# Performance work log

Hardware: AMD Instinct MI355X
Metric: run time of the kernel (lower is better)

The kernel has to match this reference:

```python
import jax, jax.numpy as jnp
import numpy as np


def setup_inputs() -> dict:
    key = jax.random.key(0)
    kq, kk, kv = jax.random.split(key, 3)
    B, H, T, D = 2, 8, 8192, 64
    return {
        "Q": jax.random.normal(kq, (B, H, T, D), dtype=jnp.float32),
        "K": jax.random.normal(kk, (B, H, T, D), dtype=jnp.float32),
        "V": jax.random.normal(kv, (B, H, T, D), dtype=jnp.float32),
        "window_size": 512,
    }


def _gather_bands(x, nb, Wn):
    # x: [B,H,T,D] -> [B,H,nb,3*Wn,D], key blocks (i-1, i, i+1) per query block i
    B, H, T, D = x.shape
    xb = x.reshape(B, H, nb, Wn, D)
    xp = jnp.pad(xb, ((0, 0), (0, 0), (1, 1), (0, 0), (0, 0)))
    return jnp.concatenate([xp[:, :, i:i + nb] for i in range(3)], axis=3)


def reference(Q, K, V, window_size):
    # Sliding-window attention: softmax over keys with |q_idx - kv_idx| <= window_size,
    # computed block-sparsely (only the 3 neighboring key blocks per query block).
    B, H, T, D = Q.shape
    Wn = int(window_size)
    assert T % Wn == 0
    nb = T // Wn
    scale = 1.0 / (D ** 0.5)

    Qb = Q.reshape(B, H, nb, Wn, D)
    Kw = _gather_bands(K, nb, Wn)  # [B,H,nb,3W,D]
    Vw = _gather_bands(V, nb, Wn)

    # scores within the band: [B,H,nb,W,3W]
    s = jnp.einsum('bhnqd,bhnkd->bhnqk', Qb, Kw) * scale

    # exact band mask: global q = n*W + q_loc, global kv = (n-1)*W + k_loc
    q_loc = jnp.arange(Wn)[:, None]
    k_loc = jnp.arange(3 * Wn)[None, :]
    band = jnp.abs(q_loc + Wn - k_loc) <= Wn          # [W, 3W]
    kv_g = (jnp.arange(nb)[:, None] - 1) * Wn + jnp.arange(3 * Wn)[None, :]  # [nb, 3W]
    valid = (kv_g >= 0) & (kv_g < T)
    mask = band[None, :, :] & valid[:, None, :]        # [nb, W, 3W]

    s = jnp.where(mask[None, None], s, -jnp.inf)
    p = jax.nn.softmax(s, axis=-1)
    o = jnp.einsum('bhnqk,bhnkd->bhnqd', p, Vw)
    return o.reshape(B, H, T, D)
```

## Files before the change

kernel.cpp:

```cpp
#include <hip/hip_runtime.h>
#include <hip/hip_bf16.h>
#include <stdint.h>

typedef __attribute__((ext_vector_type(8))) short bf16x8;
typedef __attribute__((ext_vector_type(4))) short bf16x4;
typedef __attribute__((ext_vector_type(4))) float f32x4;

#define T_SEQ   8192
#define D_HEAD  64
#define NHEADS  16
#define WIN     512
#define BQ      128
#define BK      64
#define NTILES  (T_SEQ / BK)
#define LDSR    72
#define MASKVAL (-1.0e6f)

#define WS_NEEDED ((size_t)2 * NHEADS * T_SEQ * D_HEAD * 2)

#define MFMA16(a,b,c) __builtin_amdgcn_mfma_f32_16x16x16bf16_1k(a,b,c,0,0,0)

extern "C" __device__ __attribute__((const)) float __ocml_native_exp2_f32(float);
__device__ __forceinline__ float fexp2(float x) { return __ocml_native_exp2_f32(x); }

__device__ __forceinline__ short f2bf(float f) {
    union { float f; uint32_t u; } v; v.f = f;
    return (short)((v.u + 0x7FFFu + ((v.u >> 16) & 1u)) >> 16);
}

__device__ __forceinline__ uint32_t pkbf2(float lo, float hi) {
    union { __hip_bfloat162 h; uint32_t u; } c;
    c.h = __float22bfloat162_rn(make_float2(lo, hi));
    return c.u;
}

__global__ __launch_bounds__(256, 2)
void prep_kv(const float* __restrict__ Kg, const float* __restrict__ Vg,
             short* __restrict__ Kb, short* __restrict__ Vt)
{
    __shared__ float vt[64 * 65];
    const int tid  = threadIdx.x;
    const int tile = blockIdx.x & (NTILES - 1);
    const int head = blockIdx.x >> 7;
    const size_t off = ((size_t)head * T_SEQ + (size_t)tile * BK) * D_HEAD;

    const float* ks = Kg + off;
    short* kd = Kb + off;
    #pragma unroll
    for (int i = 0; i < 4; ++i) {
        int idx = tid + 256 * i;
        float4 v = *(const float4*)(ks + idx * 4);
        short4 h = { f2bf(v.x), f2bf(v.y), f2bf(v.z), f2bf(v.w) };
        *(short4*)(kd + idx * 4) = h;
    }

    const float* vs = Vg + off;
    #pragma unroll
    for (int i = 0; i < 4; ++i) {
        int idx = tid + 256 * i;
        int row = idx >> 4, c4 = (idx & 15) << 2;
        float4 v = *(const float4*)(vs + row * D_HEAD + c4);
        *(float4*)&vt[row * 65 + c4] = v;
    }
    __syncthreads();
    short* vd = Vt + ((size_t)head * NTILES + tile) * (BK * D_HEAD);
    {
        int d = tid >> 2, kq = (tid & 3) << 4;
        short out[16];
        #pragma unroll
        for (int j = 0; j < 16; ++j) out[j] = f2bf(vt[(kq + j) * 65 + d]);
        *(bf16x8*)(vd + d * BK + kq)     = *(bf16x8*)&out[0];
        *(bf16x8*)(vd + d * BK + kq + 8) = *(bf16x8*)&out[8];
    }
}

__global__ __launch_bounds__(256, 4)
void swa_fwd(const float* __restrict__ Qg, const short* __restrict__ Kb,
             const short* __restrict__ Vt, float* __restrict__ Og)
{
    __shared__ short Ks[2][BK * LDSR];
    __shared__ short Vs[2][BK * LDSR];

    const int tid  = threadIdx.x;
    const int wave = tid >> 6;
    const int lane = tid & 63;
    const int lcol = lane & 15;
    const int quad = lane >> 4;

    const int g    = blockIdx.x;
    const int head = g >> 6;
    const int qt   = ((g & 7) << 3) | ((g >> 3) & 7);
    const int q0   = qt * BQ;
    const int tq   = q0 >> 6;

    const float* Qp = Qg + (size_t)head * T_SEQ * D_HEAD;
    const short* Kp = Kb + (size_t)head * T_SEQ * D_HEAD;
    float*       Op = Og + (size_t)head * T_SEQ * D_HEAD;

    const float qscale = 0.125f * 1.44269504088896340736f;
    const int qrow_w = q0 + wave * 32;

    bf16x8 qf[2][2];
    #pragma unroll
    for (int mt = 0; mt < 2; ++mt) {
        const float* qptr = Qp + (size_t)(qrow_w + mt*16 + lcol) * D_HEAD + quad * 8;
        #pragma unroll
        for (int ks = 0; ks < 2; ++ks) {
            float4 a = *(const float4*)(qptr + ks*32);
            float4 b = *(const float4*)(qptr + ks*32 + 4);
            bf16x8 f;
            f[0]=f2bf(a.x*qscale); f[1]=f2bf(a.y*qscale); f[2]=f2bf(a.z*qscale); f[3]=f2bf(a.w*qscale);
            f[4]=f2bf(b.x*qscale); f[5]=f2bf(b.y*qscale); f[6]=f2bf(b.z*qscale); f[7]=f2bf(b.w*qscale);
            qf[mt][ks] = f;
        }
    }

    f32x4 oacc[2][4];
    float l_run[2];
    const f32x4 zero4 = {0.f, 0.f, 0.f, 0.f};
    #pragma unroll
    for (int mt = 0; mt < 2; ++mt) {
        l_run[mt] = 0.f;
        #pragma unroll
        for (int nt = 0; nt < 4; ++nt) oacc[mt][nt] = zero4;
    }

    int t0 = (q0 - WIN) >> 6;            if (t0 < 0) t0 = 0;
    int t1 = (q0 + BQ - 1 + WIN) >> 6;   if (t1 > NTILES - 1) t1 = NTILES - 1;

    const int srow0 = tid >> 3, sc0 = (tid & 7) << 3;
    const int srow1 = srow0 + 32;
    const int sOff0 = srow0 * LDSR + sc0;
    const int sOff1 = srow1 * LDSR + sc0;

    {
        const short* ksrc = Kp + (size_t)t0 * BK * D_HEAD;
        const short* vsrc = Vt + ((size_t)head * NTILES + t0) * (BK * D_HEAD);
        *(bf16x8*)&Ks[0][sOff0] = *(const bf16x8*)(ksrc + tid * 8);
        *(bf16x8*)&Ks[0][sOff1] = *(const bf16x8*)(ksrc + (tid + 256) * 8);
        *(bf16x8*)&Vs[0][sOff0] = *(const bf16x8*)(vsrc + tid * 8);
        *(bf16x8*)&Vs[0][sOff1] = *(const bf16x8*)(vsrc + (tid + 256) * 8);
    }
    bf16x8 k0, k1, v0, v1;
    {
        const int tn = (t0 + 1 <= t1) ? t0 + 1 : t1;
        const short* ksrc = Kp + (size_t)tn * BK * D_HEAD;
        const short* vsrc = Vt + ((size_t)head * NTILES + tn) * (BK * D_HEAD);
        k0 = *(const bf16x8*)(ksrc + tid * 8);
        k1 = *(const bf16x8*)(ksrc + (tid + 256) * 8);
        v0 = *(const bf16x8*)(vsrc + tid * 8);
        v1 = *(const bf16x8*)(vsrc + (tid + 256) * 8);
    }
    __syncthreads();

    int p = 0;
    for (int t = t0; t <= t1; ++t) {
        *(bf16x8*)&Ks[p^1][sOff0] = k0;
        *(bf16x8*)&Ks[p^1][sOff1] = k1;
        *(bf16x8*)&Vs[p^1][sOff0] = v0;
        *(bf16x8*)&Vs[p^1][sOff1] = v1;

        {
            const int tn = (t + 2 <= t1) ? t + 2 : t1;
            const short* ksrc = Kp + (size_t)tn * BK * D_HEAD;
            const short* vsrc = Vt + ((size_t)head * NTILES + tn) * (BK * D_HEAD);
            k0 = *(const bf16x8*)(ksrc + tid * 8);
            k1 = *(const bf16x8*)(ksrc + (tid + 256) * 8);
            v0 = *(const bf16x8*)(vsrc + tid * 8);
            v1 = *(const bf16x8*)(vsrc + (tid + 256) * 8);
        }

        const short* Kcur = Ks[p];
        const short* Vcur = Vs[p];
        const bool edge = (t < tq - 6) || (t > tq + 7);

        #pragma unroll
        for (int h = 0; h < 2; ++h) {
            f32x4 sc[2][2];
            #pragma unroll
            for (int j = 0; j < 2; ++j) { sc[j][0] = zero4; sc[j][1] = zero4; }
            #pragma unroll
            for (int ks = 0; ks < 2; ++ks) {
                #pragma unroll
                for (int j = 0; j < 2; ++j) {
                    bf16x8 kf = *(const bf16x8*)&Kcur[((2*h+j)*16 + lcol)*LDSR + ks*32 + quad*8];
                    sc[j][0] = __builtin_amdgcn_mfma_f32_16x16x32_bf16(kf, qf[0][ks], sc[j][0], 0,0,0);
                    sc[j][1] = __builtin_amdgcn_mfma_f32_16x16x32_bf16(kf, qf[1][ks], sc[j][1], 0,0,0);
                }
            }

            if (edge) {
                #pragma unroll
                for (int j = 0; j < 2; ++j) {
                    const int kg0 = t*BK + (2*h+j)*16 + quad*4;
                    #pragma unroll
                    for (int mt = 0; mt < 2; ++mt) {
                        const int qg = qrow_w + mt*16 + lcol;
                        #pragma unroll
                        for (int r = 0; r < 4; ++r) {
                            int dq = qg - (kg0 + r);
                            if (dq > WIN || dq < -WIN) sc[j][mt][r] = MASKVAL;
                        }
                    }
                }
            }

            #pragma unroll
            for (int j = 0; j < 2; ++j) {
                const int kt = 2*h + j;
                bf16x4 vf[4];
                #pragma unroll
                for (int nt = 0; nt < 4; ++nt)
                    vf[nt] = *(const bf16x4*)&Vcur[(nt*16 + lcol)*LDSR + kt*16 + quad*4];
                #pragma unroll
                for (int mt = 0; mt < 2; ++mt) {
                    float p0 = fexp2(sc[j][mt][0]);
                    float p1 = fexp2(sc[j][mt][1]);
                    float p2 = fexp2(sc[j][mt][2]);
                    float p3 = fexp2(sc[j][mt][3]);
                    l_run[mt] += (p0 + p1) + (p2 + p3);
                    union { int2 i; bf16x4 v; } pf;
                    pf.i = make_int2((int)pkbf2(p0, p1), (int)pkbf2(p2, p3));
                    #pragma unroll
                    for (int nt = 0; nt < 4; ++nt)
                        oacc[mt][nt] = MFMA16(vf[nt], pf.v, oacc[mt][nt]);
                }
            }
        }

        __syncthreads();
        p ^= 1;
    }

    #pragma unroll
    for (int mt = 0; mt < 2; ++mt) {
        float l = l_run[mt];
        l += __shfl_xor(l, 16, 64);
        l += __shfl_xor(l, 32, 64);
        float inv = 1.0f / l;
        const int qg = qrow_w + mt*16 + lcol;
        float* op = Op + (size_t)qg * D_HEAD + quad*4;
        #pragma unroll
        for (int nt = 0; nt < 4; ++nt) {
            float4 o = { oacc[mt][nt][0]*inv, oacc[mt][nt][1]*inv,
                         oacc[mt][nt][2]*inv, oacc[mt][nt][3]*inv };
            *(float4*)(op + nt*16) = o;
        }
    }
}

#define BQF     128
__global__ __launch_bounds__(256, 4)
void swa_fused_fb(const float* __restrict__ Qg, const float* __restrict__ Kg,
                  const float* __restrict__ Vg, float* __restrict__ Og)
{
    __shared__ short Ksf[BK * LDSR];
    __shared__ short Vsf[D_HEAD * LDSR];
    __shared__ float Vtmp[BK * 65];

    const int tid  = threadIdx.x;
    const int wave = tid >> 6;
    const int lane = tid & 63;
    const int lcol = lane & 15;
    const int quad = lane >> 4;

    const int g    = blockIdx.x;
    const int head = g >> 6;
    const int qt   = ((g & 7) << 3) | ((g >> 3) & 7);
    const int q0   = qt * BQF;
    const int tq   = q0 >> 6;

    const size_t hoff = (size_t)head * T_SEQ * D_HEAD;
    const float* Qp = Qg + hoff;
    const float* Kp = Kg + hoff;
    const float* Vp = Vg + hoff;
    float*       Op = Og + hoff;

    const float qscale = 0.125f * 1.44269504088896340736f;
    const int qrow_w = q0 + wave * 32;

    bf16x8 qf[2][2];
    #pragma unroll
    for (int mt = 0; mt < 2; ++mt) {
        const float* qptr = Qp + (size_t)(qrow_w + mt*16 + lcol) * D_HEAD + quad * 8;
        #pragma unroll
        for (int ks = 0; ks < 2; ++ks) {
            float4 a = *(const float4*)(qptr + ks*32);
            float4 b = *(const float4*)(qptr + ks*32 + 4);
            bf16x8 f;
            f[0]=f2bf(a.x*qscale); f[1]=f2bf(a.y*qscale); f[2]=f2bf(a.z*qscale); f[3]=f2bf(a.w*qscale);
            f[4]=f2bf(b.x*qscale); f[5]=f2bf(b.y*qscale); f[6]=f2bf(b.z*qscale); f[7]=f2bf(b.w*qscale);
            qf[mt][ks] = f;
        }
    }

    f32x4 oacc[2][4];
    float l_run[2];
    const f32x4 zero4 = {0.f, 0.f, 0.f, 0.f};
    #pragma unroll
    for (int mt = 0; mt < 2; ++mt) {
        l_run[mt] = 0.f;
        #pragma unroll
        for (int nt = 0; nt < 4; ++nt) oacc[mt][nt] = zero4;
    }

    int t0 = (q0 - WIN) >> 6;            if (t0 < 0) t0 = 0;
    int t1 = (q0 + BQF - 1 + WIN) >> 6;  if (t1 > NTILES - 1) t1 = NTILES - 1;

    const int krow0 = tid >> 3, kc = (tid & 7) << 3;
    const int krow1 = krow0 + 32;
    const int vrow  = tid >> 4, vc = (tid & 15) << 2;
    const int td    = tid >> 2, tkq = (tid & 3) << 4;

    for (int t = t0; t <= t1; ++t) {
        const float* ksrc = Kp + (size_t)t * BK * D_HEAD;
        const float* vsrc = Vp + (size_t)t * BK * D_HEAD;
        float4 k00 = *(const float4*)(ksrc + krow0*D_HEAD + kc);
        float4 k01 = *(const float4*)(ksrc + krow0*D_HEAD + kc + 4);
        float4 k10 = *(const float4*)(ksrc + krow1*D_HEAD + kc);
        float4 k11 = *(const float4*)(ksrc + krow1*D_HEAD + kc + 4);
        float4 v0  = *(const float4*)(vsrc + (vrow     )*D_HEAD + vc);
        float4 v1  = *(const float4*)(vsrc + (vrow + 16)*D_HEAD + vc);
        float4 v2  = *(const float4*)(vsrc + (vrow + 32)*D_HEAD + vc);
        float4 v3  = *(const float4*)(vsrc + (vrow + 48)*D_HEAD + vc);

        __syncthreads();

        *(float4*)&Vtmp[(vrow     )*65 + vc] = v0;
        *(float4*)&Vtmp[(vrow + 16)*65 + vc] = v1;
        *(float4*)&Vtmp[(vrow + 32)*65 + vc] = v2;
        *(float4*)&Vtmp[(vrow + 48)*65 + vc] = v3;
        *(int4*)&Ksf[krow0*LDSR + kc] = make_int4((int)pkbf2(k00.x,k00.y), (int)pkbf2(k00.z,k00.w),
                                                  (int)pkbf2(k01.x,k01.y), (int)pkbf2(k01.z,k01.w));
        *(int4*)&Ksf[krow1*LDSR + kc] = make_int4((int)pkbf2(k10.x,k10.y), (int)pkbf2(k10.z,k10.w),
                                                  (int)pkbf2(k11.x,k11.y), (int)pkbf2(k11.z,k11.w));

        __syncthreads();

        {
            uint32_t w0 = pkbf2(Vtmp[(tkq+ 0)*65 + td], Vtmp[(tkq+ 1)*65 + td]);
            uint32_t w1 = pkbf2(Vtmp[(tkq+ 2)*65 + td], Vtmp[(tkq+ 3)*65 + td]);
            uint32_t w2 = pkbf2(Vtmp[(tkq+ 4)*65 + td], Vtmp[(tkq+ 5)*65 + td]);
            uint32_t w3 = pkbf2(Vtmp[(tkq+ 6)*65 + td], Vtmp[(tkq+ 7)*65 + td]);
            uint32_t w4 = pkbf2(Vtmp[(tkq+ 8)*65 + td], Vtmp[(tkq+ 9)*65 + td]);
            uint32_t w5 = pkbf2(Vtmp[(tkq+10)*65 + td], Vtmp[(tkq+11)*65 + td]);
            uint32_t w6 = pkbf2(Vtmp[(tkq+12)*65 + td], Vtmp[(tkq+13)*65 + td]);
            uint32_t w7 = pkbf2(Vtmp[(tkq+14)*65 + td], Vtmp[(tkq+15)*65 + td]);
            *(int4*)&Vsf[td*LDSR + tkq]     = make_int4((int)w0,(int)w1,(int)w2,(int)w3);
            *(int4*)&Vsf[td*LDSR + tkq + 8] = make_int4((int)w4,(int)w5,(int)w6,(int)w7);
        }

        __syncthreads();

        const bool edge = (t < tq - 6) || (t > tq + 7);

        #pragma unroll
        for (int h = 0; h < 2; ++h) {
            f32x4 sc[2][2];
            #pragma unroll
            for (int j = 0; j < 2; ++j) { sc[j][0] = zero4; sc[j][1] = zero4; }
            #pragma unroll
            for (int ks = 0; ks < 2; ++ks) {
                #pragma unroll
                for (int j = 0; j < 2; ++j) {
                    bf16x8 kf = *(const bf16x8*)&Ksf[((2*h+j)*16 + lcol)*LDSR + ks*32 + quad*8];
                    sc[j][0] = __builtin_amdgcn_mfma_f32_16x16x32_bf16(kf, qf[0][ks], sc[j][0], 0,0,0);
                    sc[j][1] = __builtin_amdgcn_mfma_f32_16x16x32_bf16(kf, qf[1][ks], sc[j][1], 0,0,0);
                }
            }

            if (edge) {
                #pragma unroll
                for (int j = 0; j < 2; ++j) {
                    const int kg0 = t*BK + (2*h+j)*16 + quad*4;
                    #pragma unroll
                    for (int mt = 0; mt < 2; ++mt) {
                        const int qg = qrow_w + mt*16 + lcol;
                        #pragma unroll
                        for (int r = 0; r < 4; ++r) {
                            int dq = qg - (kg0 + r);
                            if (dq > WIN || dq < -WIN) sc[j][mt][r] = MASKVAL;
                        }
                    }
                }
            }

            #pragma unroll
            for (int j = 0; j < 2; ++j) {
                const int kt = 2*h + j;
                bf16x4 vf[4];
                #pragma unroll
                for (int nt = 0; nt < 4; ++nt)
                    vf[nt] = *(const bf16x4*)&Vsf[(nt*16 + lcol)*LDSR + kt*16 + quad*4];
                #pragma unroll
                for (int mt = 0; mt < 2; ++mt) {
                    float p0 = fexp2(sc[j][mt][0]);
                    float p1 = fexp2(sc[j][mt][1]);
                    float p2 = fexp2(sc[j][mt][2]);
                    float p3 = fexp2(sc[j][mt][3]);
                    l_run[mt] += (p0 + p1) + (p2 + p3);
                    union { int2 i; bf16x4 v; } pf;
                    pf.i = make_int2((int)pkbf2(p0, p1), (int)pkbf2(p2, p3));
                    #pragma unroll
                    for (int nt = 0; nt < 4; ++nt)
                        oacc[mt][nt] = MFMA16(vf[nt], pf.v, oacc[mt][nt]);
                }
            }
        }
    }

    #pragma unroll
    for (int mt = 0; mt < 2; ++mt) {
        float l = l_run[mt];
        l += __shfl_xor(l, 16, 64);
        l += __shfl_xor(l, 32, 64);
        float inv = 1.0f / l;
        const int qg = qrow_w + mt*16 + lcol;
        float* op = Op + (size_t)qg * D_HEAD + quad*4;
        #pragma unroll
        for (int nt = 0; nt < 4; ++nt) {
            float4 o = { oacc[mt][nt][0]*inv, oacc[mt][nt][1]*inv,
                         oacc[mt][nt][2]*inv, oacc[mt][nt][3]*inv };
            *(float4*)(op + nt*16) = o;
        }
    }
}

extern "C" void kernel_launch(void* const* d_in, const int* in_sizes, int n_in,
                              void* d_out, int out_size, void* d_ws, size_t ws_size,
                              hipStream_t stream)
{
    const float* Q = (const float*)d_in[0];
    const float* K = (const float*)d_in[1];
    const float* V = (const float*)d_in[2];
    float* O = (float*)d_out;

    if (ws_size >= WS_NEEDED) {
        short* Kb = (short*)d_ws;
        short* Vt = Kb + (size_t)NHEADS * T_SEQ * D_HEAD;
        prep_kv<<<dim3(NHEADS * NTILES), dim3(256), 0, stream>>>(K, V, Kb, Vt);
        swa_fwd<<<dim3(NHEADS * (T_SEQ / BQ)), dim3(256), 0, stream>>>(Q, Kb, Vt, O);
    } else {
        swa_fused_fb<<<dim3(NHEADS * (T_SEQ / BQF)), dim3(256), 0, stream>>>(Q, K, V, O);
    }
}
```

Before: 204.5 us.

## Load K/V tiles directly into LDS with XOR-swizzled layout

Replaces the register-staged global→LDS copy of the K and V tiles with direct global_load_lds transfers, using a one-tile-ahead double-buffer pipeline. The prep kernel now writes K and V^T with an XOR swizzle on 16-byte chunks, and the LDS reads undo it. This removes the padded LDS rows while avoiding bank conflicts. The goal is to cut VGPR pressure and LDS store instructions. The risk is shallower prefetch, since distance drops from two tiles to one, plus a full vmcnt(0) wait before every barrier.

```diff
diff --git a/kernel.cpp b/kernel.cpp
--- a/kernel.cpp
+++ b/kernel.cpp
@@ -23,6 +23,10 @@
 extern "C" __device__ __attribute__((const)) float __ocml_native_exp2_f32(float);
 __device__ __forceinline__ float fexp2(float x) { return __ocml_native_exp2_f32(x); }
 
+#define GLDS16(g, l) __builtin_amdgcn_global_load_lds( \
+    (const __attribute__((address_space(1))) void*)(g), \
+    (__attribute__((address_space(3))) void*)(l), 16, 0, 0)
+
 __device__ __forceinline__ short f2bf(float f) {
     union { float f; uint32_t u; } v; v.f = f;
     return (short)((v.u + 0x7FFFu + ((v.u >> 16) & 1u)) >> 16);
@@ -47,11 +51,15 @@
     const float* ks = Kg + off;
     short* kd = Kb + off;
     #pragma unroll
-    for (int i = 0; i < 4; ++i) {
-        int idx = tid + 256 * i;
-        float4 v = *(const float4*)(ks + idx * 4);
-        short4 h = { f2bf(v.x), f2bf(v.y), f2bf(v.z), f2bf(v.w) };
-        *(short4*)(kd + idx * 4) = h;
+    for (int i = 0; i < 2; ++i) {
+        int L = tid + 256 * i;
+        int row = L >> 3, c = L & 7;
+        const float* s = ks + row * 64 + c * 8;
+        float4 a = *(const float4*)s;
+        float4 b = *(const float4*)(s + 4);
+        short out[8] = { f2bf(a.x), f2bf(a.y), f2bf(a.z), f2bf(a.w),
+                         f2bf(b.x), f2bf(b.y), f2bf(b.z), f2bf(b.w) };
+        *(bf16x8*)(kd + (row * 8 + (c ^ (row & 7))) * 8) = *(bf16x8*)out;
     }
 
     const float* vs = Vg + off;
@@ -66,11 +74,12 @@
     short* vd = Vt + ((size_t)head * NTILES + tile) * (BK * D_HEAD);
     {
         int d = tid >> 2, kq = (tid & 3) << 4;
+        int c = kq >> 3;
         short out[16];
         #pragma unroll
         for (int j = 0; j < 16; ++j) out[j] = f2bf(vt[(kq + j) * 65 + d]);
-        *(bf16x8*)(vd + d * BK + kq)     = *(bf16x8*)&out[0];
-        *(bf16x8*)(vd + d * BK + kq + 8) = *(bf16x8*)&out[8];
+        *(bf16x8*)(vd + (d * 8 + ( c      ^ (d & 7))) * 8) = *(bf16x8*)&out[0];
+        *(bf16x8*)(vd + (d * 8 + ((c + 1) ^ (d & 7))) * 8) = *(bf16x8*)&out[8];
     }
 }
 
@@ -78,14 +87,15 @@
 void swa_fwd(const float* __restrict__ Qg, const short* __restrict__ Kb,
              const short* __restrict__ Vt, float* __restrict__ Og)
 {
-    __shared__ short Ks[2][BK * LDSR];
-    __shared__ short Vs[2][BK * LDSR];
+    __shared__ short Ks[2][BK * D_HEAD];
+    __shared__ short Vs[2][BK * D_HEAD];
 
     const int tid  = threadIdx.x;
     const int wave = tid >> 6;
     const int lane = tid & 63;
     const int lcol = lane & 15;
     const int quad = lane >> 4;
+    const int rx   = lcol & 7;
 
     const int g    = blockIdx.x;
     const int head = g >> 6;
@@ -128,50 +138,35 @@
     int t0 = (q0 - WIN) >> 6;            if (t0 < 0) t0 = 0;
     int t1 = (q0 + BQ - 1 + WIN) >> 6;   if (t1 > NTILES - 1) t1 = NTILES - 1;
 
-    const int srow0 = tid >> 3, sc0 = (tid & 7) << 3;
-    const int srow1 = srow0 + 32;
-    const int sOff0 = srow0 * LDSR + sc0;
-    const int sOff1 = srow1 * LDSR + sc0;
+    const int ch0 = wave * 2, ch1 = wave * 2 + 1;
 
     {
-        const short* ksrc = Kp + (size_t)t0 * BK * D_HEAD;
+        const short* ksrc = Kp + (size_t)t0 * (BK * D_HEAD);
         const short* vsrc = Vt + ((size_t)head * NTILES + t0) * (BK * D_HEAD);
-        *(bf16x8*)&Ks[0][sOff0] = *(const bf16x8*)(ksrc + tid * 8);
-        *(bf16x8*)&Ks[0][sOff1] = *(const bf16x8*)(ksrc + (tid + 256) * 8);
-        *(bf16x8*)&Vs[0][sOff0] = *(const bf16x8*)(vsrc + tid * 8);
-        *(bf16x8*)&Vs[0][sOff1] = *(const bf16x8*)(vsrc + (tid + 256) * 8);
-    }
-    bf16x8 k0, k1, v0, v1;
-    {
-        const int tn = (t0 + 1 <= t1) ? t0 + 1 : t1;
-        const short* ksrc = Kp + (size_t)tn * BK * D_HEAD;
-        const short* vsrc = Vt + ((size_t)head * NTILES + tn) * (BK * D_HEAD);
-        k0 = *(const bf16x8*)(ksrc + tid * 8);
-        k1 = *(const bf16x8*)(ksrc + (tid + 256) * 8);
-        v0 = *(const bf16x8*)(vsrc + tid * 8);
-        v1 = *(const bf16x8*)(vsrc + (tid + 256) * 8);
-    }
+        GLDS16(ksrc + ch0*512 + lane*8, &Ks[0][ch0*512]);
+        GLDS16(ksrc + ch1*512 + lane*8, &Ks[0][ch1*512]);
+        GLDS16(vsrc + ch0*512 + lane*8, &Vs[0][ch0*512]);
+        GLDS16(vsrc + ch1*512 + lane*8, &Vs[0][ch1*512]);
+    }
+    asm volatile("s_waitcnt vmcnt(0)" ::: "memory");
     __syncthreads();
 
     int p = 0;
     for (int t = t0; t <= t1; ++t) {
-        *(bf16x8*)&Ks[p^1][sOff0] = k0;
-        *(bf16x8*)&Ks[p^1][sOff1] = k1;
-        *(bf16x8*)&Vs[p^1][sOff0] = v0;
-        *(bf16x8*)&Vs[p^1][sOff1] = v1;
-
         {
-            const int tn = (t + 2 <= t1) ? t + 2 : t1;
-            const short* ksrc = Kp + (size_t)tn * BK * D_HEAD;
+            const int tn = (t + 1 <= t1) ? t + 1 : t1;
+            const short* ksrc = Kp + (size_t)tn * (BK * D_HEAD);
             const short* vsrc = Vt + ((size_t)head * NTILES + tn) * (BK * D_HEAD);
-            k0 = *(const bf16x8*)(ksrc + tid * 8);
-            k1 = *(const bf16x8*)(ksrc + (tid + 256) * 8);
-            v0 = *(const bf16x8*)(vsrc + tid * 8);
-            v1 = *(const bf16x8*)(vsrc + (tid + 256) * 8);
-        }
-
-        const short* Kcur = Ks[p];
-        const short* Vcur = Vs[p];
+            short* kds = &Ks[p^1][0];
+            short* vds = &Vs[p^1][0];
+            GLDS16(ksrc + ch0*512 + lane*8, kds + ch0*512);
+            GLDS16(ksrc + ch1*512 + lane*8, kds + ch1*512);
+            GLDS16(vsrc + ch0*512 + lane*8, vds + ch0*512);
+            GLDS16(vsrc + ch1*512 + lane*8, vds + ch1*512);
+        }
+
+        const short* Kcur = &Ks[p][0];
+        const short* Vcur = &Vs[p][0];
         const bool edge = (t < tq - 6) || (t > tq + 7);
 
         #pragma unroll
@@ -183,7 +178,8 @@
             for (int ks = 0; ks < 2; ++ks) {
                 #pragma unroll
                 for (int j = 0; j < 2; ++j) {
-                    bf16x8 kf = *(const bf16x8*)&Kcur[((2*h+j)*16 + lcol)*LDSR + ks*32 + quad*8];
+                    bf16x8 kf = *(const bf16x8*)&Kcur[((2*h+j)*16 + lcol)*64
+                                                      + (((ks*4 + quad) ^ rx) << 3)];
                     sc[j][0] = __builtin_amdgcn_mfma_f32_16x16x32_bf16(kf, qf[0][ks], sc[j][0], 0,0,0);
                     sc[j][1] = __builtin_amdgcn_mfma_f32_16x16x32_bf16(kf, qf[1][ks], sc[j][1], 0,0,0);
                 }
@@ -211,7 +207,9 @@
                 bf16x4 vf[4];
                 #pragma unroll
                 for (int nt = 0; nt < 4; ++nt)
-                    vf[nt] = *(const bf16x4*)&Vcur[(nt*16 + lcol)*LDSR + kt*16 + quad*4];
+                    vf[nt] = *(const bf16x4*)&Vcur[(nt*16 + lcol)*64
+                                                   + (((kt*2 + (quad>>1)) ^ rx) << 3)
+                                                   + ((quad & 1) << 2)];
                 #pragma unroll
                 for (int mt = 0; mt < 2; ++mt) {
                     float p0 = fexp2(sc[j][mt][0]);
@@ -228,6 +226,7 @@
             }
         }
 
+        asm volatile("s_waitcnt vmcnt(0)" ::: "memory");
         __syncthreads();
         p ^= 1;
     }
```

After: 185.5 us. 1.1x faster.
